# Kernel tuning notes

Hardware: AMD Instinct MI355X
Metric: run time of the kernel (lower is better)

## Reference

```python
import jax, jax.numpy as jnp
import numpy as np

BITS = 4
GROUP = 128
IN = 4096
OUT = 14336
B = 64
PACK = 32 // BITS          # 8 values per int32
MAXQ = (1 << BITS) - 1     # 15


def setup_inputs() -> dict:
    key = jax.random.key(0)
    k = jax.random.split(key, 5)
    x = jax.random.normal(k[0], (B, IN), dtype=jnp.float32)
    # non-negative int32 so arithmetic right-shift behaves like logical shift
    qweight = jax.random.randint(k[1], (IN // PACK, OUT), 0, 2**31 - 1, dtype=jnp.int32)
    qzeros = jax.random.randint(k[2], (IN // GROUP, OUT // PACK), 0, 2**31 - 1, dtype=jnp.int32)
    scales = jax.random.uniform(k[3], (IN // GROUP, OUT), dtype=jnp.float32,
                                minval=1e-3, maxval=1e-2)
    bias = jax.random.normal(k[4], (OUT,), dtype=jnp.float32) * 0.01
    g_idx = (jnp.arange(IN) // GROUP).astype(jnp.int32)
    return dict(x=x, qweight=qweight, qzeros=qzeros, scales=scales, bias=bias, g_idx=g_idx)


def _dequant(qweight, qzeros, scales, g_idx):
    shifts = jnp.arange(PACK, dtype=jnp.int32) * BITS  # [PACK]
    # unpack weights: [IN//PACK, PACK, OUT] -> [IN, OUT]
    w = (qweight[:, None, :] >> shifts[None, :, None]) & MAXQ
    w = w.reshape(IN, OUT)
    # unpack zeros: [G, OUT//PACK, PACK] -> [G, OUT]; pack() stored (zeros-1), so add 1 back
    z = (qzeros[:, :, None] >> shifts[None, None, :]) & MAXQ
    z = z.reshape(-1, OUT) + 1
    # per-group dequant with arbitrary g_idx (act-order support)
    return scales[g_idx] * (w - z[g_idx]).astype(scales.dtype)


def reference(x, qweight, qzeros, scales, bias, g_idx):
    W = _dequant(qweight, qzeros, scales, g_idx)  # [IN, OUT]
    return x @ W + bias
```

## Files before the change

kernel.cpp:

```cpp
#include <hip/hip_runtime.h>
#include <hip/hip_bf16.h>

using u32 = unsigned int;
using u16 = unsigned short;

typedef __attribute__((ext_vector_type(8))) _Float16 half8;
typedef __attribute__((ext_vector_type(2))) _Float16 half2v;
typedef __attribute__((ext_vector_type(16))) float f32x16;
typedef __attribute__((ext_vector_type(4))) u32 u32x4;

#define IN_K   4096
#define OUT_N  14336
#define SPLITK 8
#define NSTAGE 4
#define OUT_ELEMS (64 * OUT_N)

__global__ __launch_bounds__(256) void prep_kernel(const float* __restrict__ x,
                                                   u16* __restrict__ xs) {
  const int t = blockIdx.x * 256 + threadIdx.x;
  const int c = t >> 6;
  const int r = t & 63;
  const float* px = x + r * IN_K + c * 8;
  const float4 a = *(const float4*)px;
  const float4 b = *(const float4*)(px + 4);
  const float af[4] = {a.x, a.y, a.z, a.w};
  const float bf[4] = {b.x, b.y, b.z, b.w};
  union { u32x4 v; u32 u[4]; } o;
#pragma unroll
  for (int i = 0; i < 4; ++i) {
    const _Float16 hl = (_Float16)af[i];
    const _Float16 hh = (_Float16)bf[i];
    u16 lo, hi;
    __builtin_memcpy(&lo, &hl, 2);
    __builtin_memcpy(&hi, &hh, 2);
    o.u[i] = (u32)lo | ((u32)hi << 16);
  }
  *(u32x4*)(xs + (size_t)t * 8) = o.v;
}

__global__ __launch_bounds__(256) void bias_init_kernel(const float* __restrict__ bias,
                                                        float* __restrict__ out) {
  const int i = (blockIdx.x * 256 + threadIdx.x) * 4;
  const int col = i % OUT_N;
  *(float4*)(out + i) = *(const float4*)(bias + col);
}

__global__ __launch_bounds__(256) void reduce_kernel(const float* __restrict__ part,
                                                     const float* __restrict__ bias,
                                                     float* __restrict__ out) {
  const int bx = blockIdx.x, ry = blockIdx.y, t = threadIdx.x;
  const int row = ry * 8 + (t >> 5);
  const int c4 = (t & 31) * 4;
  const float* p = part + (((size_t)bx * SPLITK) * 64 + row) * 128 + c4;
  float4 r = *(const float4*)(bias + bx * 128 + c4);
#pragma unroll
  for (int by = 0; by < SPLITK; ++by) {
    const float4 a = *(const float4*)(p + (size_t)by * 64 * 128);
    r.x += a.x; r.y += a.y; r.z += a.z; r.w += a.w;
  }
  *(float4*)(out + (size_t)row * OUT_N + bx * 128 + c4) = r;
}

template <bool ATOMIC>
__global__ __launch_bounds__(256, 3) void qgemm_kernel(
    const u32* __restrict__ qw, const u32* __restrict__ qz,
    const float* __restrict__ scal, const u16* __restrict__ xs,
    float* __restrict__ dst) {
  __shared__ u16 lds[2][8192];
  const int tid = threadIdx.x;
  const int lane = tid & 63;
  const int wv = tid >> 6;
  const int g = lane >> 5;
  const int nn = lane & 31;
  const int colabs = blockIdx.x * 128 + wv * 32 + nn;
  const int by = blockIdx.y;
  const int chunk0 = by * 64;
  const int grp0 = by * 4;
  const int zsh = (colabs & 7) * 4;

  f32x16 acc0, acc1;
#pragma unroll
  for (int i = 0; i < 16; ++i) { acc0[i] = 0.f; acc1[i] = 0.f; }

  auto issue = [&](int st) {
    const u16* src = xs + (size_t)(chunk0 + st * 16) * 512;
    u16* dstl = &lds[st & 1][0];
#pragma unroll
    for (int r = 0; r < 4; ++r) {
      const int p = r * 256 + tid;
      __builtin_amdgcn_global_load_lds(
          (const __attribute__((address_space(1))) void*)(src + p * 8),
          (__attribute__((address_space(3))) void*)(dstl + p * 8), 16, 0, 0);
    }
  };
  auto loadQ = [&](int st, u32* qr, float& sr, u32& zr) {
    const int c = chunk0 + st * 16;
#pragma unroll
    for (int s = 0; s < 8; ++s)
      qr[s] = qw[(size_t)(c + 2 * s + g) * OUT_N + colabs];
    sr = scal[(size_t)(grp0 + st) * OUT_N + colabs];
    zr = qz[(size_t)(grp0 + st) * (OUT_N / 8) + (colabs >> 3)];
  };

  u32 qbuf[2][8]; float sbuf[2]; u32 zbuf[2];
  issue(0);
  loadQ(0, qbuf[0], sbuf[0], zbuf[0]);
  loadQ(1, qbuf[1], sbuf[1], zbuf[1]);

#pragma unroll
  for (int st = 0; st < NSTAGE; ++st) {
    if (st < NSTAGE - 1) {
      __builtin_amdgcn_s_barrier();
      asm volatile("" ::: "memory");
      issue(st + 1);
      if (st < NSTAGE - 2)
        asm volatile("s_waitcnt vmcnt(14)" ::: "memory");
      else
        asm volatile("s_waitcnt vmcnt(4)" ::: "memory");
    } else {
      asm volatile("s_waitcnt vmcnt(0)" ::: "memory");
    }
    __builtin_amdgcn_s_barrier();
    asm volatile("" ::: "memory");

    u32 qc[8];
#pragma unroll
    for (int s = 0; s < 8; ++s) qc[s] = qbuf[st & 1][s];
    const float scur = sbuf[st & 1];
    const u32 zcur = zbuf[st & 1];
    if (st < NSTAGE - 2)
      loadQ(st + 2, qbuf[st & 1], sbuf[st & 1], zbuf[st & 1]);

    const u32 zq = (zcur >> zsh) & 0xFu;
    const u32 hzu = 0x64016401u + zq * 0x00010001u;
    half2v hz; __builtin_memcpy(&hz, &hzu, 4);
    const _Float16 hs = (_Float16)scur;
    const half2v s2 = {hs, hs};

    const u16* buf = &lds[st & 1][0];
    __builtin_amdgcn_s_setprio(1);
#pragma unroll
    for (int s = 0; s < 8; ++s) {
      const int cl = s * 2 + g;
      const half8 a0 = *(const half8*)(buf + (cl * 64 + nn) * 8);
      const half8 a1 = *(const half8*)(buf + (cl * 64 + nn + 32) * 8);
      const u32 q = qc[s];
      const u32 p0 = (q & 0x000F000Fu) | 0x64006400u;
      const u32 p1 = ((q >> 4) & 0x000F000Fu) | 0x64006400u;
      const u32 p2 = ((q >> 8) & 0x000F000Fu) | 0x64006400u;
      const u32 p3 = ((q >> 12) & 0x000F000Fu) | 0x64006400u;
      half2v t0, t1, t2, t3;
      __builtin_memcpy(&t0, &p0, 4);
      __builtin_memcpy(&t1, &p1, 4);
      __builtin_memcpy(&t2, &p2, 4);
      __builtin_memcpy(&t3, &p3, 4);
      union { half8 v; half2v h[4]; } bb;
      bb.h[0] = (t0 - hz) * s2;
      bb.h[1] = (t1 - hz) * s2;
      bb.h[2] = (t2 - hz) * s2;
      bb.h[3] = (t3 - hz) * s2;
      acc0 = __builtin_amdgcn_mfma_f32_32x32x16_f16(a0, bb.v, acc0, 0, 0, 0);
      acc1 = __builtin_amdgcn_mfma_f32_32x32x16_f16(a1, bb.v, acc1, 0, 0, 0);
    }
    __builtin_amdgcn_s_setprio(0);
  }

#pragma unroll
  for (int r = 0; r < 16; ++r) {
    const int row = (r & 3) + 8 * (r >> 2) + 4 * g;
    if (ATOMIC) {
      unsafeAtomicAdd(&dst[(size_t)row * OUT_N + colabs], acc0[r]);
      unsafeAtomicAdd(&dst[(size_t)(row + 32) * OUT_N + colabs], acc1[r]);
    } else {
      float* p = dst + (((size_t)blockIdx.x * SPLITK + by) * 64) * 128
                     + wv * 32 + nn;
      p[(size_t)row * 128] = acc0[r];
      p[(size_t)(row + 32) * 128] = acc1[r];
    }
  }
}

extern "C" void kernel_launch(void* const* d_in, const int* in_sizes, int n_in,
                              void* d_out, int out_size, void* d_ws, size_t ws_size,
                              hipStream_t stream) {
  (void)in_sizes; (void)n_in; (void)out_size;
  const float* x    = (const float*)d_in[0];
  const u32*   qw   = (const u32*)d_in[1];
  const u32*   qz   = (const u32*)d_in[2];
  const float* sc   = (const float*)d_in[3];
  const float* bias = (const float*)d_in[4];
  float* out = (float*)d_out;

  const size_t XS_BYTES   = (size_t)64 * IN_K * 2;
  const size_t PART_BYTES = (size_t)SPLITK * OUT_ELEMS * 4;
  u16* xs = (u16*)d_ws;

  prep_kernel<<<128, 256, 0, stream>>>(x, xs);

  if (ws_size >= XS_BYTES + PART_BYTES) {
    float* part = (float*)((char*)d_ws + XS_BYTES);
    qgemm_kernel<false><<<dim3(112, SPLITK), 256, 0, stream>>>(qw, qz, sc, xs, part);
    reduce_kernel<<<dim3(112, 8), 256, 0, stream>>>(part, bias, out);
  } else {
    bias_init_kernel<<<896, 256, 0, stream>>>(bias, out);
    qgemm_kernel<true><<<dim3(112, SPLITK), 256, 0, stream>>>(qw, qz, sc, xs, out);
  }
}
```

Measured before the change: 32.68 us.

## Stage packed weights through LDS and halve split-K with deeper pipeline

After: 28.78 us. -11.9%, faster.

```diff
diff --git a/kernel.cpp b/kernel.cpp
--- a/kernel.cpp
+++ b/kernel.cpp
@@ -11,8 +11,8 @@
 
 #define IN_K   4096
 #define OUT_N  14336
-#define SPLITK 8
-#define NSTAGE 4
+#define SPLITK 4
+#define NSTAGE 8
 #define OUT_ELEMS (64 * OUT_N)
 
 __global__ __launch_bounds__(256) void prep_kernel(const float* __restrict__ x,
@@ -62,89 +62,91 @@
 }
 
 template <bool ATOMIC>
-__global__ __launch_bounds__(256, 3) void qgemm_kernel(
+__global__ __launch_bounds__(256, 2) void qgemm_kernel(
     const u32* __restrict__ qw, const u32* __restrict__ qz,
     const float* __restrict__ scal, const u16* __restrict__ xs,
     float* __restrict__ dst) {
-  __shared__ u16 lds[2][8192];
+  __shared__ u16 alds[2][8192];
+  __shared__ u32 qlds[2][2048];
   const int tid = threadIdx.x;
   const int lane = tid & 63;
   const int wv = tid >> 6;
   const int g = lane >> 5;
   const int nn = lane & 31;
-  const int colabs = blockIdx.x * 128 + wv * 32 + nn;
+  const int bx = blockIdx.x;
   const int by = blockIdx.y;
-  const int chunk0 = by * 64;
-  const int grp0 = by * 4;
+  const int colabs = bx * 128 + wv * 32 + nn;
+  const int chunk0 = by * 128;
+  const int grp0 = by * NSTAGE;
   const int zsh = (colabs & 7) * 4;
 
   f32x16 acc0, acc1;
 #pragma unroll
   for (int i = 0; i < 16; ++i) { acc0[i] = 0.f; acc1[i] = 0.f; }
 
+  float sv[NSTAGE]; u32 zv[NSTAGE];
+#pragma unroll
+  for (int t = 0; t < NSTAGE; ++t) {
+    sv[t] = scal[(size_t)(grp0 + t) * OUT_N + colabs];
+    zv[t] = qz[(size_t)(grp0 + t) * (OUT_N / 8) + (colabs >> 3)];
+  }
+
   auto issue = [&](int st) {
-    const u16* src = xs + (size_t)(chunk0 + st * 16) * 512;
-    u16* dstl = &lds[st & 1][0];
+    const u16* asrc = xs + (size_t)(chunk0 + st * 16) * 512;
+    u16* adst = &alds[st & 1][0];
 #pragma unroll
     for (int r = 0; r < 4; ++r) {
       const int p = r * 256 + tid;
       __builtin_amdgcn_global_load_lds(
-          (const __attribute__((address_space(1))) void*)(src + p * 8),
-          (__attribute__((address_space(3))) void*)(dstl + p * 8), 16, 0, 0);
+          (const __attribute__((address_space(1))) void*)(asrc + p * 8),
+          (__attribute__((address_space(3))) void*)(adst + p * 8), 16, 0, 0);
+    }
+    u32* qdst = &qlds[st & 1][0];
+#pragma unroll
+    for (int r = 0; r < 2; ++r) {
+      const int p = r * 256 + tid;
+      const int j = p >> 5;
+      const int cg = p & 31;
+      const u32* src = qw + (size_t)(chunk0 + st * 16 + j) * OUT_N
+                          + bx * 128 + cg * 4;
+      __builtin_amdgcn_global_load_lds(
+          (const __attribute__((address_space(1))) void*)src,
+          (__attribute__((address_space(3))) void*)(qdst + p * 4), 16, 0, 0);
     }
   };
-  auto loadQ = [&](int st, u32* qr, float& sr, u32& zr) {
-    const int c = chunk0 + st * 16;
-#pragma unroll
-    for (int s = 0; s < 8; ++s)
-      qr[s] = qw[(size_t)(c + 2 * s + g) * OUT_N + colabs];
-    sr = scal[(size_t)(grp0 + st) * OUT_N + colabs];
-    zr = qz[(size_t)(grp0 + st) * (OUT_N / 8) + (colabs >> 3)];
-  };
-
-  u32 qbuf[2][8]; float sbuf[2]; u32 zbuf[2];
+
   issue(0);
-  loadQ(0, qbuf[0], sbuf[0], zbuf[0]);
-  loadQ(1, qbuf[1], sbuf[1], zbuf[1]);
 
 #pragma unroll
   for (int st = 0; st < NSTAGE; ++st) {
-    if (st < NSTAGE - 1) {
+    if (st == 0) {
+      issue(1);
+      asm volatile("s_waitcnt vmcnt(6)" ::: "memory");
+    } else if (st < NSTAGE - 1) {
       __builtin_amdgcn_s_barrier();
-      asm volatile("" ::: "memory");
       issue(st + 1);
-      if (st < NSTAGE - 2)
-        asm volatile("s_waitcnt vmcnt(14)" ::: "memory");
-      else
-        asm volatile("s_waitcnt vmcnt(4)" ::: "memory");
+      asm volatile("s_waitcnt vmcnt(6)" ::: "memory");
     } else {
+      __builtin_amdgcn_s_barrier();
       asm volatile("s_waitcnt vmcnt(0)" ::: "memory");
     }
     __builtin_amdgcn_s_barrier();
     asm volatile("" ::: "memory");
 
-    u32 qc[8];
-#pragma unroll
-    for (int s = 0; s < 8; ++s) qc[s] = qbuf[st & 1][s];
-    const float scur = sbuf[st & 1];
-    const u32 zcur = zbuf[st & 1];
-    if (st < NSTAGE - 2)
-      loadQ(st + 2, qbuf[st & 1], sbuf[st & 1], zbuf[st & 1]);
-
-    const u32 zq = (zcur >> zsh) & 0xFu;
+    const u32 zq = (zv[st] >> zsh) & 0xFu;
     const u32 hzu = 0x64016401u + zq * 0x00010001u;
     half2v hz; __builtin_memcpy(&hz, &hzu, 4);
-    const _Float16 hs = (_Float16)scur;
+    const _Float16 hs = (_Float16)sv[st];
     const half2v s2 = {hs, hs};
 
-    const u16* buf = &lds[st & 1][0];
-    __builtin_amdgcn_s_setprio(1);
+    const u16* abuf = &alds[st & 1][0];
+    const u32* qbuf = &qlds[st & 1][0];
 #pragma unroll
     for (int s = 0; s < 8; ++s) {
       const int cl = s * 2 + g;
-      const half8 a0 = *(const half8*)(buf + (cl * 64 + nn) * 8);
-      const half8 a1 = *(const half8*)(buf + (cl * 64 + nn + 32) * 8);
-      const u32 q = qc[s];
+      const half8 a0 = *(const half8*)(abuf + (cl * 64 + nn) * 8);
+      const half8 a1 = *(const half8*)(abuf + (cl * 64 + nn + 32) * 8);
+      const u32 q = qbuf[cl * 128 + wv * 32 + nn];
       const u32 p0 = (q & 0x000F000Fu) | 0x64006400u;
       const u32 p1 = ((q >> 4) & 0x000F000Fu) | 0x64006400u;
       const u32 p2 = ((q >> 8) & 0x000F000Fu) | 0x64006400u;
@@ -162,7 +164,6 @@
       acc0 = __builtin_amdgcn_mfma_f32_32x32x16_f16(a0, bb.v, acc0, 0, 0, 0);
       acc1 = __builtin_amdgcn_mfma_f32_32x32x16_f16(a1, bb.v, acc1, 0, 0, 0);
     }
-    __builtin_amdgcn_s_setprio(0);
   }
 
 #pragma unroll
@@ -172,8 +173,7 @@
       unsafeAtomicAdd(&dst[(size_t)row * OUT_N + colabs], acc0[r]);
       unsafeAtomicAdd(&dst[(size_t)(row + 32) * OUT_N + colabs], acc1[r]);
     } else {
-      float* p = dst + (((size_t)blockIdx.x * SPLITK + by) * 64) * 128
-                     + wv * 32 + nn;
+      float* p = dst + (((size_t)bx * SPLITK + by) * 64) * 128 + wv * 32 + nn;
       p[(size_t)row * 128] = acc0[r];
       p[(size_t)(row + 32) * 128] = acc1[r];
     }
@@ -192,7 +192,7 @@
   float* out = (float*)d_out;
 
   const size_t XS_BYTES   = (size_t)64 * IN_K * 2;
-  const size_t PART_BYTES = (size_t)SPLITK * OUT_ELEMS * 4;
+  const size_t PART_BYTES = (size_t)SPLITK * 112 * 8192 * 4;
   u16* xs = (u16*)d_ws;
 
   prep_kernel<<<128, 256, 0, stream>>>(x, xs);
```
